# Optimization experiments

Measured on AMD Instinct MI355X. Metric: run time of the kernel, lower is better.

Reference implementation:

```python
import jax, jax.numpy as jnp
import numpy as np

B, C, T, V = 8, 64, 16, 207
H, WSZ = 8, 4
EPS = 1e-5


def setup_inputs() -> dict:
    key = jax.random.key(0)
    ks = jax.random.split(key, 16)
    def w(k, shape):
        return jax.random.normal(k, shape, jnp.float32) * 0.02
    inp = {"x": jax.random.normal(ks[0], (B, C, T, V), jnp.float32)}
    for i, s in enumerate("ab"):
        o = 1 + i * 4
        inp[f"qkv_w_{s}"] = w(ks[o], (C, 3 * C))
        inp[f"qkv_b_{s}"] = jnp.zeros((3 * C,), jnp.float32)
        inp[f"proj_w_{s}"] = w(ks[o + 1], (C, C))
        inp[f"proj_b_{s}"] = jnp.zeros((C,), jnp.float32)
        inp[f"ffn_w1_{s}"] = w(ks[o + 2], (C, 4 * C))
        inp[f"ffn_b1_{s}"] = jnp.zeros((4 * C,), jnp.float32)
        inp[f"ffn_w2_{s}"] = w(ks[o + 3], (4 * C, C))
        inp[f"ffn_b2_{s}"] = jnp.zeros((C,), jnp.float32)
        inp[f"ln_{s}1_g"] = jnp.ones((C, T, V), jnp.float32)
        inp[f"ln_{s}1_b"] = jnp.zeros((C, T, V), jnp.float32)
        inp[f"ln_{s}2_g"] = jnp.ones((C, T, V), jnp.float32)
        inp[f"ln_{s}2_b"] = jnp.zeros((C, T, V), jnp.float32)
    inp["n_head"] = H
    inp["window_size"] = WSZ
    return inp


def _layer_norm(x, g, b):
    # LayerNorm over (C, T, V) dims of [B, C, T, V]
    mu = jnp.mean(x, axis=(1, 2, 3), keepdims=True)
    var = jnp.var(x, axis=(1, 2, 3), keepdims=True)
    return (x - mu) / jnp.sqrt(var + EPS) * g + b


def _window_att(x, wqkv, bqkv, wo, bo, n_head, wsz):
    # Joint spatio-temporal attention within windows of `wsz` timesteps.
    b_, c_, t_, v_ = x.shape
    nw = t_ // wsz
    dh = c_ // n_head
    # [B,C,T,V] -> [B,T,V,C] -> [B,nW, wsz*V, C]
    xt = jnp.transpose(x, (0, 2, 3, 1)).reshape(b_, nw, wsz * v_, c_)
    qkv = xt @ wqkv + bqkv  # [B,nW,N,3C]
    q, k, v = jnp.split(qkv, 3, axis=-1)
    def heads(t):
        return t.reshape(b_, nw, -1, n_head, dh).transpose(0, 1, 3, 2, 4)  # [B,nW,H,N,dh]
    q, k, v = heads(q), heads(k), heads(v)
    scale = 1.0 / jnp.sqrt(jnp.asarray(dh, jnp.float32))
    att = jax.nn.softmax(jnp.einsum('bwhnd,bwhmd->bwhnm', q, k) * scale, axis=-1)
    out = jnp.einsum('bwhnm,bwhmd->bwhnd', att, v)
    out = out.transpose(0, 1, 3, 2, 4).reshape(b_, nw, wsz * v_, c_) @ wo + bo
    return out.reshape(b_, t_, v_, c_).transpose(0, 3, 1, 2)


def _ffn(x, w1, b1, w2, b2):
    h = jax.nn.relu(jnp.einsum('bctv,cd->bdtv', x, w1) + b1[None, :, None, None])
    return jnp.einsum('bdtv,dc->bctv', h, w2) + b2[None, :, None, None]


def _block(x, wqkv, bqkv, wo, bo, w1, b1, w2, b2, g1, be1, g2, be2, n_head, wsz):
    x = _window_att(x, wqkv, bqkv, wo, bo, n_head, wsz) + x
    x = _layer_norm(x, g1, be1)
    x = _ffn(x, w1, b1, w2, b2) + x
    x = _layer_norm(x, g2, be2)
    # cyclic shift along time by shift_pixel = wsz // 2
    return jnp.roll(x, -(wsz // 2), axis=2)


def reference(x, qkv_w_a, qkv_b_a, proj_w_a, proj_b_a, ffn_w1_a, ffn_b1_a, ffn_w2_a, ffn_b2_a,
              ln_a1_g, ln_a1_b, ln_a2_g, ln_a2_b,
              qkv_w_b, qkv_b_b, proj_w_b, proj_b_b, ffn_w1_b, ffn_b1_b, ffn_w2_b, ffn_b2_b,
              ln_b1_g, ln_b1_b, ln_b2_g, ln_b2_b, n_head, window_size):
    x = _block(x, qkv_w_a, qkv_b_a, proj_w_a, proj_b_a, ffn_w1_a, ffn_b1_a, ffn_w2_a, ffn_b2_a,
               ln_a1_g, ln_a1_b, ln_a2_g, ln_a2_b, n_head, window_size)
    x = _block(x, qkv_w_b, qkv_b_b, proj_w_b, proj_b_b, ffn_w1_b, ffn_b1_b, ffn_w2_b, ffn_b2_b,
               ln_b1_g, ln_b1_b, ln_b2_g, ln_b2_b, n_head, window_size)
    return x
```

## Files before the change

kernel.cpp:

```cpp
#include <hip/hip_runtime.h>
#include <hip/hip_bf16.h>

#define Bb  8
#define Cc  64
#define Tt  16
#define Vv  207
#define Hh  8
#define DH  8
#define NW  4
#define WSZ 4
#define Nn  (WSZ*Vv)
#define TV  (Tt*Vv)
#define CTV (Cc*Tt*Vv)
#define S   (Bb*CTV)
#define NBWH (Bb*NW*Hh)
#define EPSF 1e-5f
#define QSCALE 0.51006971401146f
#define FRAG_BWH (52*64*4)

typedef __attribute__((ext_vector_type(4))) short bf16x4;
typedef __attribute__((ext_vector_type(4))) float f32x4;
typedef __attribute__((ext_vector_type(2))) unsigned int u32x2;
typedef __attribute__((ext_vector_type(4))) unsigned int u32x4;

static __device__ __forceinline__ short f2bf(float f) {
    union { float f; unsigned u; } v; v.f = f;
    unsigned r = (v.u + 0x7FFFu + ((v.u >> 16) & 1u)) >> 16;
    return (short)r;
}

static __device__ __forceinline__ bf16x4 pack4(float a, float b, float c, float d) {
    unsigned ua = __builtin_bit_cast(unsigned, a) + 0x8000u;
    unsigned ub = __builtin_bit_cast(unsigned, b) + 0x8000u;
    unsigned uc = __builtin_bit_cast(unsigned, c) + 0x8000u;
    unsigned ud = __builtin_bit_cast(unsigned, d) + 0x8000u;
    u32x2 t;
    t[0] = (ua >> 16) | (ub & 0xFFFF0000u);
    t[1] = (uc >> 16) | (ud & 0xFFFF0000u);
    return __builtin_bit_cast(bf16x4, t);
}

static __device__ __forceinline__ bf16x4 pack4_trunc(float a, float b, float c, float d) {
    unsigned ea = __builtin_bit_cast(unsigned, a);
    unsigned eb = __builtin_bit_cast(unsigned, b);
    unsigned ec = __builtin_bit_cast(unsigned, c);
    unsigned ed = __builtin_bit_cast(unsigned, d);
    u32x2 t;
    t[0] = __builtin_amdgcn_perm(eb, ea, 0x07060302u);
    t[1] = __builtin_amdgcn_perm(ed, ec, 0x07060302u);
    return __builtin_bit_cast(bf16x4, t);
}

__global__ __launch_bounds__(512) void qkv_kernel(const float* __restrict__ src,
        const float* __restrict__ st, const float* __restrict__ g, const float* __restrict__ be,
        const float* __restrict__ qw, const float* __restrict__ bias,
        short* __restrict__ qf, short* __restrict__ kf, short* __restrict__ vf,
        float* __restrict__ stats, int doInit) {
    __shared__ short wqs[12288];
    __shared__ float bqs[192];
    __shared__ short os[64*196];
    int tid = threadIdx.x;
    int b = blockIdx.x / 52;
    int r0 = (blockIdx.x % 52) * 64;
    const float* xb = src + (size_t)b*CTV;

    int lane = tid & 63; int wv = tid >> 6;
    int rs = wv & 3; int gsel = wv >> 2;
    int l15 = lane & 15; int quad = lane >> 4;
    int r = r0 + rs*16 + l15;
    int rc = (r < TV) ? r : TV-1;
    int t = rc / Vv; int vv = rc - t*Vv;
    float mean = 0.f, rstd = 0.f; int off;
    if (st) {
        mean = st[b*2] * (1.0f/CTV);
        float var = st[b*2+1] * (1.0f/CTV) - mean*mean;
        rstd = rsqrtf(var + EPSF);
        off = ((t+2)&15)*Vv + vv;
    } else off = rc;

    bf16x4 xf[4];
    #pragma unroll
    for (int kc = 0; kc < 4; ++kc) {
        #pragma unroll
        for (int j = 0; j < 4; ++j) {
            int idx = (kc*16 + quad*4 + j)*TV + off;
            float x0 = xb[idx];
            if (st) x0 = (x0 - mean)*rstd*g[idx] + be[idx];
            xf[kc][j] = f2bf(x0);
        }
    }

    for (int fs = tid; fs < 3072; fs += 512) {
        int nt = fs >> 8; int kc = (fs >> 6) & 3; int ln = fs & 63;
        int li = ln & 15; int q = ln >> 4;
        bf16x4 o;
        #pragma unroll
        for (int j = 0; j < 4; ++j) o[j] = f2bf(qw[(kc*16 + q*4 + j)*192 + nt*16 + li]);
        *((bf16x4*)&wqs[fs*4]) = o;
    }
    if (tid < 192) bqs[tid] = bias[tid];

    if (doInit) {
        if (blockIdx.x == 0 && tid < 64) stats[tid] = 0.f;
        for (int i = blockIdx.x*512 + tid; i < NBWH*1664; i += 416*512) {
            int bwh = i / 1664; int rest = i % 1664;
            int nt = rest >> 5; int u = rest & 31;
            size_t base = (size_t)bwh*FRAG_BWH + nt*256;
            *((u32x2*)&qf[base + (32+u)*4]) = (u32x2){0u, 0u};
            *((u32x2*)&kf[base + (32+u)*4]) = (u32x2){0u, 0u};
            int vlane = (u>>3)*16 + 8 + (u&7);
            short v = ((u&7) == 0) ? (short)0x3F80 : (short)0;
            bf16x4 vv4 = {v,v,v,v};
            *((bf16x4*)&vf[base + vlane*4]) = vv4;
            if (nt == 51) {
                bf16x4 z4 = {0,0,0,0};
                if (u < 4) {
                    *((bf16x4*)&kf[base + (12+u)*4]) = z4;
                    *((bf16x4*)&qf[base + (12+u)*4]) = z4;
                } else if (u < 8) {
                    *((bf16x4*)&kf[base + (24+u)*4]) = z4;
                    *((bf16x4*)&qf[base + (24+u)*4]) = z4;
                } else if (u < 16) {
                    *((bf16x4*)&vf[base + (40+u)*4]) = z4;
                }
            }
        }
    }
    __syncthreads();

    f32x4 accv[6];
    #pragma unroll
    for (int ntl = 0; ntl < 6; ++ntl) {
        int nt = gsel*6 + ntl;
        float4 bb = *((const float4*)&bqs[nt*16 + quad*4]);
        f32x4 acc = {bb.x, bb.y, bb.z, bb.w};
        #pragma unroll
        for (int kc = 0; kc < 4; ++kc) {
            bf16x4 wf2 = *((const bf16x4*)&wqs[((nt*4 + kc)*64 + lane)*4]);
            acc = __builtin_amdgcn_mfma_f32_16x16x16bf16_1k(wf2, xf[kc], acc, 0, 0, 0);
        }
        accv[ntl] = acc;
    }

    int pos = rs*16 + l15;
    #pragma unroll
    for (int ntl = 0; ntl < 6; ++ntl) {
        int nt = gsel*6 + ntl;
        f32x4 a = accv[ntl];
        bf16x4 pk = (nt < 4) ? pack4(a[0]*QSCALE, a[1]*QSCALE, a[2]*QSCALE, a[3]*QSCALE)
                             : pack4(a[0], a[1], a[2], a[3]);
        *((bf16x4*)&os[pos*196 + nt*16 + quad*4]) = pk;
    }
    __syncthreads();

    int pp = tid & 63;
    int rr = r0 + pp;
    bool pv = rr < TV;
    int rrc = pv ? rr : TV-1;
    int t4 = rrc / Vv; int vv4 = rrc - t4*Vv;
    int n2 = (t4 & 3)*Vv + vv4;
    int nt2 = n2 >> 4; int l15n = n2 & 15;
    int wbase = (b*NW + (t4 >> 2))*Hh;
    if (pv) {
        int h = wv;
        size_t fb = ((size_t)(wbase+h)*52 + nt2)*256;
        bf16x4 q0 = *((const bf16x4*)&os[pp*196 + h*8]);
        bf16x4 q1 = *((const bf16x4*)&os[pp*196 + h*8 + 4]);
        *((bf16x4*)&qf[fb + l15n*4])        = q0;
        *((bf16x4*)&qf[fb + (16 + l15n)*4]) = q1;
        bf16x4 k0 = *((const bf16x4*)&os[pp*196 + 64 + h*8]);
        bf16x4 k1 = *((const bf16x4*)&os[pp*196 + 64 + h*8 + 4]);
        *((bf16x4*)&kf[fb + l15n*4])        = k0;
        *((bf16x4*)&kf[fb + (16 + l15n)*4]) = k1;
    }
    #pragma unroll
    for (int u2 = 0; u2 < 2; ++u2) {
        int unit = u2*512 + tid;
        int rq = unit >> 6;
        int hd = unit & 63;
        int r4 = r0 + rq*4;
        if (r4 < TV) {
            int w = r4 / Nn;
            int n = r4 - w*Nn;
            int nt2v = n >> 4; int quadv = (n >> 2) & 3;
            int h = hd >> 3; int d = hd & 7;
            int posb = rq*4;
            bf16x4 vo;
            vo[0] = os[(posb+0)*196 + 128 + hd];
            vo[1] = os[(posb+1)*196 + 128 + hd];
            vo[2] = os[(posb+2)*196 + 128 + hd];
            vo[3] = os[(posb+3)*196 + 128 + hd];
            *((bf16x4*)&vf[((((size_t)(b*NW + w)*Hh + h)*52 + nt2v)*64 + quadv*16 + d)*4]) = vo;
        }
    }
}

__global__ __launch_bounds__(1024) void attn_kernel(const short* __restrict__ qf,
        const short* __restrict__ kf, const short* __restrict__ vf,
        short* __restrict__ att) {
    __shared__ short ks2[FRAG_BWH];
    __shared__ short vs2[FRAG_BWH];
    int bwh = blockIdx.x;
    int tid = threadIdx.x;
    int lane = tid & 63;
    int wv = tid >> 6;
    int quad = lane >> 4;
    int l15 = lane & 15;

    {
        const u32x4* kg = (const u32x4*)(kf + (size_t)bwh*FRAG_BWH);
        const u32x4* vg = (const u32x4*)(vf + (size_t)bwh*FRAG_BWH);
        u32x4* kd = (u32x4*)ks2; u32x4* vd = (u32x4*)vs2;
        for (int idx = tid; idx < 1664; idx += 1024) { kd[idx] = kg[idx]; vd[idx] = vg[idx]; }
    }
    __syncthreads();

    int nm = (wv < 4) ? 4 : 3;
    const short* qbase = qf + (size_t)bwh*FRAG_BWH;
    bf16x4 aq[4];
    f32x4 oacc[4];
    #pragma unroll
    for (int i = 0; i < 4; ++i) {
        aq[i] = (bf16x4){0,0,0,0};
        oacc[i] = (f32x4){0.f,0.f,0.f,0.f};
        if (i < nm)
            aq[i] = *(const bf16x4*)(qbase + ((wv + 16*i)*256 + lane*4));
    }

    #pragma unroll 1
    for (int nt = 0; nt < 52; ++nt) {
        bf16x4 ak = *(const bf16x4*)&ks2[nt*256 + lane*4];
        bf16x4 av = *(const bf16x4*)&vs2[nt*256 + lane*4];
        bool mask = (nt == 51) && (quad == 3);
        #pragma unroll
        for (int i = 0; i < 4; ++i) {
            if (i < nm) {
                f32x4 s = __builtin_amdgcn_mfma_f32_16x16x16bf16_1k(
                              ak, aq[i], (f32x4){0.f,0.f,0.f,0.f}, 0, 0, 0);
                bf16x4 pb = pack4_trunc(__builtin_amdgcn_exp2f(s[0]), __builtin_amdgcn_exp2f(s[1]),
                                        __builtin_amdgcn_exp2f(s[2]), __builtin_amdgcn_exp2f(s[3]));
                if (mask) pb = (bf16x4){0,0,0,0};
                oacc[i] = __builtin_amdgcn_mfma_f32_16x16x16bf16_1k(av, pb, oacc[i], 0, 0, 0);
            }
        }
    }
    int h = bwh & 7; int bw = bwh >> 3;
    #pragma unroll
    for (int i = 0; i < 4; ++i) {
        if (i < nm) {
            float ls = __shfl(oacc[i][0], 32 + l15, 64);
            float inv = 1.f / ls;
            int m = (wv + 16*i)*16 + l15;
            if (quad < 2 && m < Nn) {
                bf16x4 ov = pack4(oacc[i][0]*inv, oacc[i][1]*inv,
                                  oacc[i][2]*inv, oacc[i][3]*inv);
                *((bf16x4*)&att[((size_t)bw*Nn + m)*Cc + h*DH + quad*4]) = ov;
            }
        }
    }
}

__global__ __launch_bounds__(512) void proj_kernel(const short* __restrict__ att,
        const float* __restrict__ pw, const float* __restrict__ bo,
        const float* __restrict__ resid,
        const float* __restrict__ st, const float* __restrict__ g, const float* __restrict__ be,
        float* __restrict__ out, float* __restrict__ stats) {
    __shared__ short wos[4096];
    __shared__ float bos[64];
    __shared__ float r1[512], r2[512];
    int tid = threadIdx.x;
    int b = blockIdx.x / 52;
    int r0 = (blockIdx.x % 52) * 64;
    const float* xb = resid + (size_t)b*CTV;

    int lane = tid & 63; int wv = tid >> 6;
    int rs = wv & 3; int gsel = wv >> 2;
    int l15 = lane & 15; int quad = lane >> 4;
    int r = r0 + rs*16 + l15;
    bool valid = r < TV;
    int rc = valid ? r : TV-1;
    int t = rc / Vv; int vv = rc - t*Vv;
    int n = (t & 3)*Vv + vv;
    int bw = b*NW + (t >> 2);
    const short* arow = att + ((size_t)bw*Nn + n)*Cc;
    bf16x4 af[4];
    #pragma unroll
    for (int kc = 0; kc < 4; ++kc)
        af[kc] = *((const bf16x4*)&arow[kc*16 + quad*4]);

    for (int fs = tid; fs < 1024; fs += 512) {
        int nt = fs >> 8; int kc = (fs >> 6) & 3; int ln = fs & 63;
        int li = ln & 15; int q = ln >> 4;
        bf16x4 o;
        #pragma unroll
        for (int j = 0; j < 4; ++j) o[j] = f2bf(pw[(kc*16 + q*4 + j)*64 + nt*16 + li]);
        *((bf16x4*)&wos[fs*4]) = o;
    }
    if (tid < 64) bos[tid] = bo[tid];
    __syncthreads();

    f32x4 acc[2];
    #pragma unroll
    for (int ntl = 0; ntl < 2; ++ntl) {
        int nt = gsel*2 + ntl;
        float4 bb = *((const float4*)&bos[nt*16 + quad*4]);
        acc[ntl] = (f32x4){bb.x, bb.y, bb.z, bb.w};
        #pragma unroll
        for (int kc = 0; kc < 4; ++kc) {
            bf16x4 wf2 = *((const bf16x4*)&wos[((nt*4 + kc)*64 + lane)*4]);
            acc[ntl] = __builtin_amdgcn_mfma_f32_16x16x16bf16_1k(wf2, af[kc], acc[ntl], 0, 0, 0);
        }
    }
    float mean = 0.f, rstd = 0.f; int off;
    if (st) {
        mean = st[b*2] * (1.0f/CTV);
        float var = st[b*2+1] * (1.0f/CTV) - mean*mean;
        rstd = rsqrtf(var + EPSF);
        off = ((t+2)&15)*Vv + vv;
    } else off = rc;
    float s1 = 0.f, s2 = 0.f;
    if (valid) {
        #pragma unroll
        for (int ntl = 0; ntl < 2; ++ntl) {
            int nt = gsel*2 + ntl;
            #pragma unroll
            for (int j = 0; j < 4; ++j) {
                int c_out = nt*16 + quad*4 + j;
                int ridx = c_out*TV + off;
                float xv = xb[ridx];
                if (st) xv = (xv - mean)*rstd*g[ridx] + be[ridx];
                float val = acc[ntl][j] + xv;
                out[(size_t)b*CTV + (size_t)c_out*TV + r] = val;
                s1 += val; s2 += val*val;
            }
        }
    }
    r1[tid] = s1; r2[tid] = s2;
    __syncthreads();
    for (int o = 256; o > 0; o >>= 1) {
        if (tid < o) { r1[tid] += r1[tid+o]; r2[tid] += r2[tid+o]; }
        __syncthreads();
    }
    if (tid == 0) { atomicAdd(&stats[b*2], r1[0]); atomicAdd(&stats[b*2+1], r2[0]); }
}

__global__ void ln_apply_kernel(const float* __restrict__ x,
                                const float* __restrict__ g,
                                const float* __restrict__ be,
                                const float* __restrict__ stats,
                                float* __restrict__ out) {
    int i4 = (blockIdx.x*256 + threadIdx.x) * 4;
    if (i4 >= S) return;
    int b = i4 / CTV; int r = i4 % CTV;
    int c = r / TV; int q2 = r % TV; int t = q2 / Vv; int vv = q2 - t*Vv;
    float mean = stats[b*2] * (1.0f/CTV);
    float var  = stats[b*2+1] * (1.0f/CTV) - mean*mean;
    float rstd = rsqrtf(var + EPSF);
    float4 xv = *((const float4*)&x[i4]);
    float vals[4] = {xv.x, xv.y, xv.z, xv.w};
    size_t obase = (size_t)(b*Cc + c)*Tt;
    #pragma unroll
    for (int j = 0; j < 4; ++j) {
        float val = (vals[j]-mean)*rstd*g[r+j] + be[r+j];
        int tout = (t - 2 + Tt) & 15;
        out[(obase + tout)*Vv + vv] = val;
        if (++vv == Vv) { vv = 0; ++t; }
    }
}

__global__ __launch_bounds__(512) void ffn_kernel(const float* __restrict__ xin,
        const float* __restrict__ st, const float* __restrict__ g, const float* __restrict__ be,
        const float* __restrict__ w1r, const float* __restrict__ b1,
        const float* __restrict__ w2r, const float* __restrict__ b2,
        float* __restrict__ out, float* __restrict__ stats) {
    __shared__ short w1s[16384];
    __shared__ short w2s[16384];
    __shared__ short xsf[4096];
    __shared__ float b1s[256];
    __shared__ float b2s[64];
    __shared__ float r1s[512], r2s[512];
    int tid = threadIdx.x;
    int b = blockIdx.x / 52;
    int r0 = (blockIdx.x % 52) * 64;
    const float* xb = xin + (size_t)b*CTV;
    float mean = st[b*2] * (1.0f/CTV);
    float var  = st[b*2+1] * (1.0f/CTV) - mean*mean;
    float rstd = rsqrtf(var + EPSF);

    for (int s2 = tid; s2 < 1024; s2 += 512) {
        int wv2 = s2 >> 8; int kc = (s2 >> 6) & 3; int ln = s2 & 63;
        int l15 = ln & 15; int quad = ln >> 4;
        int r = r0 + wv2*16 + l15; if (r >= TV) r = TV-1;
        bf16x4 f;
        #pragma unroll
        for (int j = 0; j < 4; ++j) {
            int idx = (kc*16 + quad*4 + j)*TV + r;
            f[j] = f2bf((xb[idx] - mean)*rstd*g[idx] + be[idx]);
        }
        *((bf16x4*)&xsf[s2*4]) = f;
    }
    for (int fs = tid; fs < 4096; fs += 512) {
        int nt = fs >> 8; int kc = (fs >> 6) & 3; int ln = fs & 63;
        int li = ln & 15; int q = ln >> 4;
        bf16x4 o1;
        #pragma unroll
        for (int j = 0; j < 4; ++j) o1[j] = f2bf(w1r[(kc*16 + q*4 + j)*256 + nt*16 + li]);
        *((bf16x4*)&w1s[fs*4]) = o1;
        bf16x4 o2;
        #pragma unroll
        for (int j = 0; j < 4; ++j) o2[j] = f2bf(w2r[(nt*16 + q*4 + j)*64 + kc*16 + li]);
        *((bf16x4*)&w2s[fs*4]) = o2;
    }
    if (tid < 256) b1s[tid] = b1[tid];
    if (tid < 64) b2s[tid] = b2[tid];
    __syncthreads();

    int lane = tid & 63; int wv = tid >> 6;
    int rs = wv & 3; int gsel = wv >> 2;
    int l15 = lane & 15; int quad = lane >> 4;
    bf16x4 xf[4];
    #pragma unroll
    for (int kc = 0; kc < 4; ++kc)
        xf[kc] = *((const bf16x4*)&xsf[((rs*4 + kc)*64 + lane)*4]);

    f32x4 oacc[2];
    #pragma unroll
    for (int ctl = 0; ctl < 2; ++ctl) oacc[ctl] = (f32x4){0.f,0.f,0.f,0.f};

    for (int nt = 0; nt < 16; ++nt) {
        float4 bb = *((const float4*)&b1s[nt*16 + quad*4]);
        f32x4 acc = {bb.x, bb.y, bb.z, bb.w};
        #pragma unroll
        for (int kc = 0; kc < 4; ++kc) {
            bf16x4 wfv = *((const bf16x4*)&w1s[((nt*4 + kc)*64 + lane)*4]);
            acc = __builtin_amdgcn_mfma_f32_16x16x16bf16_1k(wfv, xf[kc], acc, 0, 0, 0);
        }
        bf16x4 pf = pack4(fmaxf(acc[0], 0.f), fmaxf(acc[1], 0.f),
                          fmaxf(acc[2], 0.f), fmaxf(acc[3], 0.f));
        #pragma unroll
        for (int ctl = 0; ctl < 2; ++ctl) {
            int ct = gsel*2 + ctl;
            bf16x4 wfv2 = *((const bf16x4*)&w2s[((nt*4 + ct)*64 + lane)*4]);
            oacc[ctl] = __builtin_amdgcn_mfma_f32_16x16x16bf16_1k(wfv2, pf, oacc[ctl], 0, 0, 0);
        }
    }
    int r = r0 + rs*16 + l15;
    float s1 = 0.f, s2v = 0.f;
    if (r < TV) {
        #pragma unroll
        for (int ctl = 0; ctl < 2; ++ctl) {
            int ct = gsel*2 + ctl;
            #pragma unroll
            for (int j = 0; j < 4; ++j) {
                int c_out = ct*16 + quad*4 + j;
                int idx = c_out*TV + r;
                float xv = (xb[idx] - mean)*rstd*g[idx] + be[idx];
                float val = oacc[ctl][j] + b2s[c_out] + xv;
                out[(size_t)b*CTV + idx] = val;
                s1 += val; s2v += val*val;
            }
        }
    }
    r1s[tid] = s1; r2s[tid] = s2v;
    __syncthreads();
    for (int o = 256; o > 0; o >>= 1) {
        if (tid < o) { r1s[tid] += r1s[tid+o]; r2s[tid] += r2s[tid+o]; }
        __syncthreads();
    }
    if (tid == 0) { atomicAdd(&stats[b*2], r1s[0]); atomicAdd(&stats[b*2+1], r2s[0]); }
}

extern "C" void kernel_launch(void* const* d_in, const int* in_sizes, int n_in,
                              void* d_out, int out_size, void* d_ws, size_t ws_size,
                              hipStream_t stream) {
    const float* xin = (const float*)d_in[0];

    float* bufA  = (float*)d_ws;
    float* bufB  = bufA + S;
    float* stats = bufB + S;
    short* qf    = (short*)(stats + 64);
    short* kf    = qf + (size_t)NBWH*FRAG_BWH;
    short* vf    = kf + (size_t)NBWH*FRAG_BWH;
    short* att   = vf + (size_t)NBWH*FRAG_BWH;

    const float* A0  = (const float*)d_in[1];
    const float* A1  = (const float*)d_in[2];
    const float* A2  = (const float*)d_in[3];
    const float* A3  = (const float*)d_in[4];
    const float* A4  = (const float*)d_in[5];
    const float* A5  = (const float*)d_in[6];
    const float* A6  = (const float*)d_in[7];
    const float* A7  = (const float*)d_in[8];
    const float* A8  = (const float*)d_in[9];
    const float* A9  = (const float*)d_in[10];
    const float* A10 = (const float*)d_in[11];
    const float* A11 = (const float*)d_in[12];
    const float* B0  = (const float*)d_in[13];
    const float* B1  = (const float*)d_in[14];
    const float* B2  = (const float*)d_in[15];
    const float* B3  = (const float*)d_in[16];
    const float* B4  = (const float*)d_in[17];
    const float* B5  = (const float*)d_in[18];
    const float* B6  = (const float*)d_in[19];
    const float* B7  = (const float*)d_in[20];
    const float* B8  = (const float*)d_in[21];
    const float* B9  = (const float*)d_in[22];
    const float* B10 = (const float*)d_in[23];
    const float* B11 = (const float*)d_in[24];

    float* st1a = stats + 0;
    float* st2a = stats + 16;
    float* st1b = stats + 32;
    float* st2b = stats + 48;

    qkv_kernel<<<Bb*52, 512, 0, stream>>>(xin, nullptr, nullptr, nullptr,
                                          A0, A1, qf, kf, vf, stats, 1);
    attn_kernel<<<NBWH, 1024, 0, stream>>>(qf, kf, vf, att);
    proj_kernel<<<Bb*52, 512, 0, stream>>>(att, A2, A3, xin,
                                           nullptr, nullptr, nullptr, bufB, st1a);
    ffn_kernel<<<Bb*52, 512, 0, stream>>>(bufB, st1a, A8, A9,
                                          A4, A5, A6, A7, bufB, st2a);
    qkv_kernel<<<Bb*52, 512, 0, stream>>>(bufB, st2a, A10, A11,
                                          B0, B1, qf, kf, vf, stats, 0);
    attn_kernel<<<NBWH, 1024, 0, stream>>>(qf, kf, vf, att);
    proj_kernel<<<Bb*52, 512, 0, stream>>>(att, B2, B3, bufB,
                                           st2a, A10, A11, bufA, st1b);
    ffn_kernel<<<Bb*52, 512, 0, stream>>>(bufA, st1b, B8, B9,
                                          B4, B5, B6, B7, bufA, st2b);
    ln_apply_kernel<<<(S/4+255)/256, 256, 0, stream>>>(bufA, B10, B11, st2b, (float*)d_out);
}
```

Before: 273.2 us.

## Pre-convert all weights to bf16 MFMA fragments once and read them from global memory

The first qkv launch now converts every later weight matrix (proj, FFN, qkv of block B) into bf16 MFMA fragment layout in a workspace buffer. Proj, FFN and the second qkv kernel then read fragments straight from global memory instead of each block re-converting fp32 weights into shared memory. This removes redundant per-block conversion, a barrier and a large LDS footprint, which may raise occupancy. The cost is extra work in the first kernel and uncoalesced-ish global/L2 reads of the weights inside the MFMA loops.

```diff
diff --git a/kernel.cpp b/kernel.cpp
--- a/kernel.cpp
+++ b/kernel.cpp
@@ -17,6 +17,7 @@
 #define EPSF 1e-5f
 #define QSCALE 0.51006971401146f
 #define FRAG_BWH (52*64*4)
+#define WFU 21504
 
 typedef __attribute__((ext_vector_type(4))) short bf16x4;
 typedef __attribute__((ext_vector_type(4))) float f32x4;
@@ -51,13 +52,19 @@
     return __builtin_bit_cast(bf16x4, t);
 }
 
+template<bool LA>
 __global__ __launch_bounds__(512) void qkv_kernel(const float* __restrict__ src,
         const float* __restrict__ st, const float* __restrict__ g, const float* __restrict__ be,
-        const float* __restrict__ qw, const float* __restrict__ bias,
+        const float* __restrict__ qw,
+        const short* __restrict__ wfq,
+        const float* __restrict__ bias,
         short* __restrict__ qf, short* __restrict__ kf, short* __restrict__ vf,
-        float* __restrict__ stats, int doInit) {
-    __shared__ short wqs[12288];
-    __shared__ float bqs[192];
+        float* __restrict__ stats,
+        const float* __restrict__ pA, const float* __restrict__ w1A, const float* __restrict__ w2A,
+        const float* __restrict__ qwB, const float* __restrict__ pB,
+        const float* __restrict__ w1B, const float* __restrict__ w2B,
+        short* __restrict__ wfg) {
+    __shared__ short wqs[LA ? 12288 : 64];
     __shared__ short os[64*196];
     int tid = threadIdx.x;
     int b = blockIdx.x / 52;
@@ -71,7 +78,7 @@
     int rc = (r < TV) ? r : TV-1;
     int t = rc / Vv; int vv = rc - t*Vv;
     float mean = 0.f, rstd = 0.f; int off;
-    if (st) {
+    if (!LA) {
         mean = st[b*2] * (1.0f/CTV);
         float var = st[b*2+1] * (1.0f/CTV) - mean*mean;
         rstd = rsqrtf(var + EPSF);
@@ -85,23 +92,44 @@
         for (int j = 0; j < 4; ++j) {
             int idx = (kc*16 + quad*4 + j)*TV + off;
             float x0 = xb[idx];
-            if (st) x0 = (x0 - mean)*rstd*g[idx] + be[idx];
+            if (!LA) x0 = (x0 - mean)*rstd*g[idx] + be[idx];
             xf[kc][j] = f2bf(x0);
         }
     }
 
-    for (int fs = tid; fs < 3072; fs += 512) {
-        int nt = fs >> 8; int kc = (fs >> 6) & 3; int ln = fs & 63;
-        int li = ln & 15; int q = ln >> 4;
-        bf16x4 o;
-        #pragma unroll
-        for (int j = 0; j < 4; ++j) o[j] = f2bf(qw[(kc*16 + q*4 + j)*192 + nt*16 + li]);
-        *((bf16x4*)&wqs[fs*4]) = o;
-    }
-    if (tid < 192) bqs[tid] = bias[tid];
-
-    if (doInit) {
+    if constexpr (LA) {
+        for (int fs = tid; fs < 3072; fs += 512) {
+            int nt = fs >> 8; int kc = (fs >> 6) & 3; int ln = fs & 63;
+            int li = ln & 15; int q = ln >> 4;
+            bf16x4 o;
+            #pragma unroll
+            for (int j = 0; j < 4; ++j) o[j] = f2bf(qw[(kc*16 + q*4 + j)*192 + nt*16 + li]);
+            *((bf16x4*)&wqs[fs*4]) = o;
+        }
         if (blockIdx.x == 0 && tid < 64) stats[tid] = 0.f;
+        for (int i = blockIdx.x*512 + tid; i < WFU; i += 416*512) {
+            int s, kind; const float* sp;
+            if (i < 1024)       { s = i;        sp = pA;  kind = 0; }
+            else if (i < 5120)  { s = i-1024;   sp = w1A; kind = 1; }
+            else if (i < 9216)  { s = i-5120;   sp = w2A; kind = 2; }
+            else if (i < 12288) { s = i-9216;   sp = qwB; kind = 3; }
+            else if (i < 13312) { s = i-12288;  sp = pB;  kind = 0; }
+            else if (i < 17408) { s = i-13312;  sp = w1B; kind = 1; }
+            else                { s = i-17408;  sp = w2B; kind = 2; }
+            int nt = s >> 8; int kc = (s >> 6) & 3; int ln = s & 63;
+            int li = ln & 15; int q = ln >> 4;
+            bf16x4 o;
+            #pragma unroll
+            for (int j = 0; j < 4; ++j) {
+                int sidx;
+                if (kind == 0)      sidx = (kc*16 + q*4 + j)*64  + nt*16 + li;
+                else if (kind == 1) sidx = (kc*16 + q*4 + j)*256 + nt*16 + li;
+                else if (kind == 2) sidx = (nt*16 + q*4 + j)*64  + kc*16 + li;
+                else                sidx = (kc*16 + q*4 + j)*192 + nt*16 + li;
+                o[j] = f2bf(sp[sidx]);
+            }
+            *((bf16x4*)&wfg[i*4]) = o;
+        }
         for (int i = blockIdx.x*512 + tid; i < NBWH*1664; i += 416*512) {
             int bwh = i / 1664; int rest = i % 1664;
             int nt = rest >> 5; int u = rest & 31;
@@ -125,18 +153,20 @@
                 }
             }
         }
-    }
-    __syncthreads();
+        __syncthreads();
+    }
 
     f32x4 accv[6];
     #pragma unroll
     for (int ntl = 0; ntl < 6; ++ntl) {
         int nt = gsel*6 + ntl;
-        float4 bb = *((const float4*)&bqs[nt*16 + quad*4]);
+        float4 bb = *((const float4*)&bias[nt*16 + quad*4]);
         f32x4 acc = {bb.x, bb.y, bb.z, bb.w};
         #pragma unroll
         for (int kc = 0; kc < 4; ++kc) {
-            bf16x4 wf2 = *((const bf16x4*)&wqs[((nt*4 + kc)*64 + lane)*4]);
+            bf16x4 wf2;
+            if constexpr (LA) wf2 = *((const bf16x4*)&wqs[((nt*4 + kc)*64 + lane)*4]);
+            else              wf2 = *((const bf16x4*)&wfq[((size_t)((nt*4 + kc)*64 + lane))*4]);
             acc = __builtin_amdgcn_mfma_f32_16x16x16bf16_1k(wf2, xf[kc], acc, 0, 0, 0);
         }
         accv[ntl] = acc;
@@ -261,12 +291,10 @@
 }
 
 __global__ __launch_bounds__(512) void proj_kernel(const short* __restrict__ att,
-        const float* __restrict__ pw, const float* __restrict__ bo,
+        const short* __restrict__ wfp, const float* __restrict__ bo,
         const float* __restrict__ resid,
         const float* __restrict__ st, const float* __restrict__ g, const float* __restrict__ be,
         float* __restrict__ out, float* __restrict__ stats) {
-    __shared__ short wos[4096];
-    __shared__ float bos[64];
     __shared__ float r1[512], r2[512];
     int tid = threadIdx.x;
     int b = blockIdx.x / 52;
@@ -288,26 +316,15 @@
     for (int kc = 0; kc < 4; ++kc)
         af[kc] = *((const bf16x4*)&arow[kc*16 + quad*4]);
 
-    for (int fs = tid; fs < 1024; fs += 512) {
-        int nt = fs >> 8; int kc = (fs >> 6) & 3; int ln = fs & 63;
-        int li = ln & 15; int q = ln >> 4;
-        bf16x4 o;
-        #pragma unroll
-        for (int j = 0; j < 4; ++j) o[j] = f2bf(pw[(kc*16 + q*4 + j)*64 + nt*16 + li]);
-        *((bf16x4*)&wos[fs*4]) = o;
-    }
-    if (tid < 64) bos[tid] = bo[tid];
-    __syncthreads();
-
     f32x4 acc[2];
     #pragma unroll
     for (int ntl = 0; ntl < 2; ++ntl) {
         int nt = gsel*2 + ntl;
-        float4 bb = *((const float4*)&bos[nt*16 + quad*4]);
+        float4 bb = *((const float4*)&bo[nt*16 + quad*4]);
         acc[ntl] = (f32x4){bb.x, bb.y, bb.z, bb.w};
         #pragma unroll
         for (int kc = 0; kc < 4; ++kc) {
-            bf16x4 wf2 = *((const bf16x4*)&wos[((nt*4 + kc)*64 + lane)*4]);
+            bf16x4 wf2 = *((const bf16x4*)&wfp[((size_t)((nt*4 + kc)*64 + lane))*4]);
             acc[ntl] = __builtin_amdgcn_mfma_f32_16x16x16bf16_1k(wf2, af[kc], acc[ntl], 0, 0, 0);
         }
     }
@@ -370,14 +387,10 @@
 
 __global__ __launch_bounds__(512) void ffn_kernel(const float* __restrict__ xin,
         const float* __restrict__ st, const float* __restrict__ g, const float* __restrict__ be,
-        const float* __restrict__ w1r, const float* __restrict__ b1,
-        const float* __restrict__ w2r, const float* __restrict__ b2,
+        const short* __restrict__ wf1g, const float* __restrict__ b1,
+        const short* __restrict__ wf2g, const float* __restrict__ b2,
         float* __restrict__ out, float* __restrict__ stats) {
-    __shared__ short w1s[16384];
-    __shared__ short w2s[16384];
     __shared__ short xsf[4096];
-    __shared__ float b1s[256];
-    __shared__ float b2s[64];
     __shared__ float r1s[512], r2s[512];
     int tid = threadIdx.x;
     int b = blockIdx.x / 52;
@@ -399,20 +412,6 @@
         }
         *((bf16x4*)&xsf[s2*4]) = f;
     }
-    for (int fs = tid; fs < 4096; fs += 512) {
-        int nt = fs >> 8; int kc = (fs >> 6) & 3; int ln = fs & 63;
-        int li = ln & 15; int q = ln >> 4;
-        bf16x4 o1;
-        #pragma unroll
-        for (int j = 0; j < 4; ++j) o1[j] = f2bf(w1r[(kc*16 + q*4 + j)*256 + nt*16 + li]);
-        *((bf16x4*)&w1s[fs*4]) = o1;
-        bf16x4 o2;
-        #pragma unroll
-        for (int j = 0; j < 4; ++j) o2[j] = f2bf(w2r[(nt*16 + q*4 + j)*64 + kc*16 + li]);
-        *((bf16x4*)&w2s[fs*4]) = o2;
-    }
-    if (tid < 256) b1s[tid] = b1[tid];
-    if (tid < 64) b2s[tid] = b2[tid];
     __syncthreads();
 
     int lane = tid & 63; int wv = tid >> 6;
@@ -428,11 +427,11 @@
     for (int ctl = 0; ctl < 2; ++ctl) oacc[ctl] = (f32x4){0.f,0.f,0.f,0.f};
 
     for (int nt = 0; nt < 16; ++nt) {
-        float4 bb = *((const float4*)&b1s[nt*16 + quad*4]);
+        float4 bb = *((const float4*)&b1[nt*16 + quad*4]);
         f32x4 acc = {bb.x, bb.y, bb.z, bb.w};
         #pragma unroll
         for (int kc = 0; kc < 4; ++kc) {
-            bf16x4 wfv = *((const bf16x4*)&w1s[((nt*4 + kc)*64 + lane)*4]);
+            bf16x4 wfv = *((const bf16x4*)&wf1g[((size_t)((nt*4 + kc)*64 + lane))*4]);
             acc = __builtin_amdgcn_mfma_f32_16x16x16bf16_1k(wfv, xf[kc], acc, 0, 0, 0);
         }
         bf16x4 pf = pack4(fmaxf(acc[0], 0.f), fmaxf(acc[1], 0.f),
@@ -440,7 +439,7 @@
         #pragma unroll
         for (int ctl = 0; ctl < 2; ++ctl) {
             int ct = gsel*2 + ctl;
-            bf16x4 wfv2 = *((const bf16x4*)&w2s[((nt*4 + ct)*64 + lane)*4]);
+            bf16x4 wfv2 = *((const bf16x4*)&wf2g[((size_t)((nt*4 + ct)*64 + lane))*4]);
             oacc[ctl] = __builtin_amdgcn_mfma_f32_16x16x16bf16_1k(wfv2, pf, oacc[ctl], 0, 0, 0);
         }
     }
@@ -455,7 +454,7 @@
                 int c_out = ct*16 + quad*4 + j;
                 int idx = c_out*TV + r;
                 float xv = (xb[idx] - mean)*rstd*g[idx] + be[idx];
-                float val = oacc[ctl][j] + b2s[c_out] + xv;
+                float val = oacc[ctl][j] + b2[c_out] + xv;
                 out[(size_t)b*CTV + idx] = val;
                 s1 += val; s2v += val*val;
             }
@@ -482,6 +481,7 @@
     short* kf    = qf + (size_t)NBWH*FRAG_BWH;
     short* vf    = kf + (size_t)NBWH*FRAG_BWH;
     short* att   = vf + (size_t)NBWH*FRAG_BWH;
+    short* wfg   = att + (size_t)32*Nn*64;
 
     const float* A0  = (const float*)d_in[1];
     const float* A1  = (const float*)d_in[2];
@@ -513,19 +513,30 @@
     float* st1b = stats + 32;
     float* st2b = stats + 48;
 
-    qkv_kernel<<<Bb*52, 512, 0, stream>>>(xin, nullptr, nullptr, nullptr,
-                                          A0, A1, qf, kf, vf, stats, 1);
+    const short* wprojA = wfg;
+    const short* w1Ag   = wfg + 4096;
+    const short* w2Ag   = wfg + 20480;
+    const short* wqkvB  = wfg + 36864;
+    const short* wprojB = wfg + 49152;
+    const short* w1Bg   = wfg + 53248;
+    const short* w2Bg   = wfg + 69632;
+
+    qkv_kernel<true><<<Bb*52, 512, 0, stream>>>(xin, nullptr, nullptr, nullptr,
+                                          A0, nullptr, A1, qf, kf, vf, stats,
+                                          A2, A4, A6, B0, B2, B4, B6, wfg);
     attn_kernel<<<NBWH, 1024, 0, stream>>>(qf, kf, vf, att);
-    proj_kernel<<<Bb*52, 512, 0, stream>>>(att, A2, A3, xin,
+    proj_kernel<<<Bb*52, 512, 0, stream>>>(att, wprojA, A3, xin,
                                            nullptr, nullptr, nullptr, bufB, st1a);
     ffn_kernel<<<Bb*52, 512, 0, stream>>>(bufB, st1a, A8, A9,
-                                          A4, A5, A6, A7, bufB, st2a);
-    qkv_kernel<<<Bb*52, 512, 0, stream>>>(bufB, st2a, A10, A11,
-                                          B0, B1, qf, kf, vf, stats, 0);
+                                          w1Ag, A5, w2Ag, A7, bufB, st2a);
+    qkv_kernel<false><<<Bb*52, 512, 0, stream>>>(bufB, st2a, A10, A11,
+                                          nullptr, wqkvB, B1, qf, kf, vf, stats,
+                                          nullptr, nullptr, nullptr, nullptr,
+                                          nullptr, nullptr, nullptr, nullptr);
     attn_kernel<<<NBWH, 1024, 0, stream>>>(qf, kf, vf, att);
-    proj_kernel<<<Bb*52, 512, 0, stream>>>(att, B2, B3, bufB,
+    proj_kernel<<<Bb*52, 512, 0, stream>>>(att, wprojB, B3, bufB,
                                            st2a, A10, A11, bufA, st1b);
     ffn_kernel<<<Bb*52, 512, 0, stream>>>(bufA, st1b, B8, B9,
-                                          B4, B5, B6, B7, bufA, st2b);
+                                          w1Bg, B5, w2Bg, B7, bufA, st2b);
     ln_apply_kernel<<<(S/4+255)/256, 256, 0, stream>>>(bufA, B10, B11, st2b, (float*)d_out);
 }
```

New measurement: 272.6 us. Within noise of the previous version (-0.2%).
